# Kernel optimization log

Measured on AMD Instinct MI355X. Metric: run time of the kernel, lower is better.

The kernel has to match this reference:

```python
import jax, jax.numpy as jnp
import numpy as np
from jax import lax

B, C, H, W = 8, 128, 128, 128
K = 3
RED = 8

def setup_inputs() -> dict:
    key = jax.random.key(0)
    ks = jax.random.split(key, 8)
    s = 0.05
    return {
        "x": jax.random.normal(ks[0], (B, C, H, W), dtype=jnp.float32),
        "altitude": jax.random.normal(ks[1], (B, 128), dtype=jnp.float32),
        "W1": jax.random.normal(ks[2], (128, 128), dtype=jnp.float32) * s,          # Linear(128,128), no bias
        "W2": jax.random.normal(ks[3], (128 * K * K, 128), dtype=jnp.float32) * s,  # Linear(128,128*k*k)
        "conv_w": jax.random.normal(ks[4], (C, C), dtype=jnp.float32) * s,          # 1x1 conv weight [out,in]
        "conv_b": jax.random.normal(ks[5], (C,), dtype=jnp.float32) * s,
        "ca_w1": jax.random.normal(ks[6], (C // RED, C), dtype=jnp.float32) * s,    # CA squeeze 1x1 conv
        "ca_w2": jax.random.normal(ks[7], (C, C // RED), dtype=jnp.float32) * s,    # CA excite 1x1 conv
    }

def reference(x, altitude, W1, W2, conv_w, conv_b, ca_w1, ca_w2):
    b, c, h, w = x.shape
    # kernel generator MLP: [b,128] -> [b, 128*K*K] -> (b*c, 1, K, K)
    feat = jax.nn.leaky_relu(altitude @ W1.T, negative_slope=0.1)
    kern = (feat @ W2.T).reshape(b * c, 1, K, K)
    # per-sample, per-channel conv: groups = b*c (pure generated depthwise)
    pad = (K - 1) // 2
    xr = x.reshape(1, b * c, h, w)
    out = lax.conv_general_dilated(
        xr, kern, window_strides=(1, 1), padding=[(pad, pad), (pad, pad)],
        dimension_numbers=("NCHW", "OIHW", "NCHW"), feature_group_count=b * c)
    out = jax.nn.relu(out).reshape(b, c, h, w)
    # 1x1 pointwise conv
    out = jnp.einsum("bchw,oc->bohw", out, conv_w) + conv_b[None, :, None, None]
    # channel attention from altitude
    a1 = jax.nn.leaky_relu(altitude @ ca_w1.T, negative_slope=0.1)
    att = jax.nn.sigmoid(a1 @ ca_w2.T)  # [b, c]
    return out + x * att[:, :, None, None]
```

## Files before the change

kernel.cpp:

```cpp
#include <hip/hip_runtime.h>
#include <math.h>

typedef __attribute__((ext_vector_type(8))) __bf16 bf16x8;
typedef __attribute__((ext_vector_type(4))) __bf16 bf16x4;
typedef __attribute__((ext_vector_type(4))) float f32x4;

#define PLANE 16384
#define ROWW 128


__global__ __launch_bounds__(256) void precompute_kernel(
    const float* __restrict__ altitude,
    const float* __restrict__ W1,
    const float* __restrict__ W2,
    const float* __restrict__ ca_w1,
    const float* __restrict__ ca_w2,
    const float* __restrict__ conv_w,
    float* __restrict__ ws)
{
    int bid = blockIdx.x;
    int b = bid >> 2;
    int q = bid & 3;
    int t = threadIdx.x;
    __shared__ float alt_s[128];
    __shared__ float feat_s[128];
    __shared__ float a1_s[16];

    if (t < 128) alt_s[t] = altitude[b * 128 + t];
    __syncthreads();

    if (t < 128) {
        float s = 0.f;
        const float* wrow = W1 + t * 128;
        for (int j = 0; j < 128; ++j) s += alt_s[j] * wrow[j];
        feat_s[t] = (s >= 0.f) ? s : 0.1f * s;
    } else if (t < 144 && q == 1) {
        int r = t - 128;
        float s = 0.f;
        const float* wrow = ca_w1 + r * 128;
        for (int j = 0; j < 128; ++j) s += alt_s[j] * wrow[j];
        a1_s[r] = (s >= 0.f) ? s : 0.1f * s;
    }
    __syncthreads();

    for (int i = t; i < 288; i += 256) {
        int m = q * 288 + i;
        float s = 0.f;
        const float* wrow = W2 + m * 128;
        for (int j = 0; j < 128; ++j) s += feat_s[j] * wrow[j];
        int c = m / 9, k = m % 9;
        ws[b * 1536 + c * 12 + k] = s;
    }
    if (q == 1 && t < 128) {
        float s = 0.f;
        const float* wrow = ca_w2 + t * 16;
        for (int r = 0; r < 16; ++r) s += a1_s[r] * wrow[r];
        ws[12288 + b * 128 + t] = 1.f / (1.f + expf(-s));
    }
    if (q == 2 && t < 256) {
        int kc   = t >> 6;
        int lane = t & 63;
        int o  = b * 16 + (lane & 15);
        int cb = kc * 32 + 8 * (lane >> 4);
        bf16x8 v;
        #pragma unroll
        for (int j = 0; j < 8; ++j)
            v[j] = (__bf16)conv_w[o * 128 + cb + j];
        ushort* wf = (ushort*)(ws + 13312);
        *reinterpret_cast<bf16x8*>(wf + ((size_t)(b * 4 + kc) * 64 + lane) * 8) = v;
    }
}

__global__ __launch_bounds__(512, 4) void fused_kernel(
    const float* __restrict__ x,
    const float* __restrict__ conv_b,
    const float* __restrict__ ws,
    float* __restrict__ out)
{
    const float* __restrict__ kern_w = ws;
    const float* __restrict__ att_w  = ws + 12288;
    const ushort* __restrict__ wfrag = (const ushort*)(ws + 13312);

    int bid = blockIdx.x;
    int b  = bid & 7;
    int rb = bid >> 3;
    int h0 = rb * 2;

    __shared__ __align__(16) ushort dwT[2][128 * 136];
    __shared__ __align__(16) float ktaps[128 * 12];

    int t = threadIdx.x;
    const float* __restrict__ xb = x + (size_t)b * 128 * PLANE;

    for (int i = t; i < 384; i += 512) {
        float4 v = *(const float4*)(kern_w + b * 1536 + i * 4);
        *(float4*)(&ktaps[i * 4]) = v;
    }
    __syncthreads();

    {
        int pg = t & 15;
        int cg = t >> 4;
        int gp0 = pg * 8;
        int c0 = cg * 4;

        float mL = (pg > 0)  ? 1.f : 0.f;
        float mR = (pg < 15) ? 1.f : 0.f;
        float mTop = (rb > 0)  ? 1.f : 0.f;
        float mBot = (rb < 63) ? 1.f : 0.f;
        int r0 = (rb > 0)  ? h0 - 1 : h0;
        int r3 = (rb < 63) ? h0 + 2 : h0;

        bf16x4 bv[2][8];

#define NEIGH(A, B, LV, RV) \
        float LV = __shfl_up((B).w, 1) * mL; \
        float RV = __shfl_down((A).x, 1) * mR;

#define ROWACC(A, B, LV, RV, KL, KC, KR) {                                \
        o0 = fmaf((KL), LV,    fmaf((KC), (A).x, fmaf((KR), (A).y, o0))); \
        o1 = fmaf((KL), (A).x, fmaf((KC), (A).y, fmaf((KR), (A).z, o1))); \
        o2 = fmaf((KL), (A).y, fmaf((KC), (A).z, fmaf((KR), (A).w, o2))); \
        o3 = fmaf((KL), (A).z, fmaf((KC), (A).w, fmaf((KR), (B).x, o3))); \
        o4 = fmaf((KL), (A).w, fmaf((KC), (B).x, fmaf((KR), (B).y, o4))); \
        o5 = fmaf((KL), (B).x, fmaf((KC), (B).y, fmaf((KR), (B).z, o5))); \
        o6 = fmaf((KL), (B).y, fmaf((KC), (B).z, fmaf((KR), (B).w, o6))); \
        o7 = fmaf((KL), (B).z, fmaf((KC), (B).w, fmaf((KR), RV,    o7))); }

#define DW_CH(CI) {                                                    \
        const float* q_ = xb + (size_t)(c0 + (CI)) * PLANE;            \
        const float* p0_ = q_ + r0 * ROWW + gp0;                       \
        const float* p1_ = q_ + h0 * ROWW + gp0;                       \
        const float* p2_ = q_ + (h0 + 1) * ROWW + gp0;                 \
        const float* p3_ = q_ + r3 * ROWW + gp0;                       \
        float4 a0 = *(const float4*)p0_, b0 = *(const float4*)(p0_ + 4); \
        float4 a1 = *(const float4*)p1_, b1 = *(const float4*)(p1_ + 4); \
        float4 a2 = *(const float4*)p2_, b2 = *(const float4*)(p2_ + 4); \
        float4 a3 = *(const float4*)p3_, b3 = *(const float4*)(p3_ + 4); \
        NEIGH(a0, b0, l0, rr0) NEIGH(a1, b1, l1, rr1)                  \
        NEIGH(a2, b2, l2, rr2) NEIGH(a3, b3, l3, rr3)                  \
        const float* tp = ktaps + (c0 + (CI)) * 12;                    \
        float4 kA = *(const float4*)tp;                                \
        float4 kB = *(const float4*)(tp + 4);                          \
        float  k8v = tp[8];                                            \
        {            \
            float o0 = 0.f, o1 = 0.f, o2 = 0.f, o3 = 0.f;              \
            float o4 = 0.f, o5 = 0.f, o6 = 0.f, o7 = 0.f;              \
            ROWACC(a0, b0, l0, rr0, kA.x * mTop, kA.y * mTop, kA.z * mTop) \
            ROWACC(a1, b1, l1, rr1, kA.w, kB.x, kB.y)                  \
            ROWACC(a2, b2, l2, rr2, kB.z, kB.w, k8v)                   \
            bv[0][0][(CI)] = (__bf16)fmaxf(o0, 0.f);                   \
            bv[0][1][(CI)] = (__bf16)fmaxf(o1, 0.f);                   \
            bv[0][2][(CI)] = (__bf16)fmaxf(o2, 0.f);                   \
            bv[0][3][(CI)] = (__bf16)fmaxf(o3, 0.f);                   \
            bv[0][4][(CI)] = (__bf16)fmaxf(o4, 0.f);                   \
            bv[0][5][(CI)] = (__bf16)fmaxf(o5, 0.f);                   \
            bv[0][6][(CI)] = (__bf16)fmaxf(o6, 0.f);                   \
            bv[0][7][(CI)] = (__bf16)fmaxf(o7, 0.f);                   \
        }                                                              \
        {         \
            float o0 = 0.f, o1 = 0.f, o2 = 0.f, o3 = 0.f;              \
            float o4 = 0.f, o5 = 0.f, o6 = 0.f, o7 = 0.f;              \
            ROWACC(a1, b1, l1, rr1, kA.x, kA.y, kA.z)                  \
            ROWACC(a2, b2, l2, rr2, kA.w, kB.x, kB.y)                  \
            ROWACC(a3, b3, l3, rr3, kB.z * mBot, kB.w * mBot, k8v * mBot) \
            bv[1][0][(CI)] = (__bf16)fmaxf(o0, 0.f);                   \
            bv[1][1][(CI)] = (__bf16)fmaxf(o1, 0.f);                   \
            bv[1][2][(CI)] = (__bf16)fmaxf(o2, 0.f);                   \
            bv[1][3][(CI)] = (__bf16)fmaxf(o3, 0.f);                   \
            bv[1][4][(CI)] = (__bf16)fmaxf(o4, 0.f);                   \
            bv[1][5][(CI)] = (__bf16)fmaxf(o5, 0.f);                   \
            bv[1][6][(CI)] = (__bf16)fmaxf(o6, 0.f);                   \
            bv[1][7][(CI)] = (__bf16)fmaxf(o7, 0.f);                   \
        } }

        DW_CH(0) DW_CH(1) DW_CH(2) DW_CH(3)
#undef DW_CH
#undef ROWACC
#undef NEIGH

        int slotoff = (((cg >> 1) ^ pg) * 8) + ((cg & 1) * 4);
#define ST(RW, J) *reinterpret_cast<bf16x4*>(&dwT[RW][(pg * 8 + (J)) * 136 + slotoff]) = bv[RW][J];
        ST(0,0) ST(0,1) ST(0,2) ST(0,3) ST(0,4) ST(0,5) ST(0,6) ST(0,7)
        ST(1,0) ST(1,1) ST(1,2) ST(1,3) ST(1,4) ST(1,5) ST(1,6) ST(1,7)
#undef ST
    }
    __syncthreads();
    __builtin_amdgcn_sched_barrier(0);

    {
        int w    = t >> 6;
        int lane = t & 63;
        int r = lane & 15;
        int g = lane >> 4;

        bf16x8 bfr[4];
        #pragma unroll
        for (int kc = 0; kc < 4; ++kc)
            bfr[kc] = *reinterpret_cast<const bf16x8*>(
                wfrag + ((size_t)(w * 4 + kc) * 64 + lane) * 8);

        int o = w * 16 + r;
        float bi = conv_b[o];
        float at = att_w[b * 128 + o];

        #pragma unroll 1
        for (int r2 = 0; r2 < 2; ++r2) {
            const ushort* plane = dwT[r2];
            size_t rowoff = (size_t)(b * 128 + o) * PLANE + (size_t)(h0 + r2) * ROWW;
            const float* xrow = x + rowoff;
            float* orow = out + rowoff;

            float4 xv[8];
            #pragma unroll
            for (int pt = 0; pt < 8; ++pt)
                xv[pt] = *(const float4*)(xrow + pt * 16 + g * 4);

            f32x4 acc[8];
            #pragma unroll
            for (int pt = 0; pt < 8; ++pt) acc[pt] = (f32x4){0.f, 0.f, 0.f, 0.f};

            #pragma unroll
            for (int pt = 0; pt < 8; ++pt) {
                int px = pt * 16 + r;
                int srow = px * 136;
                int s2 = px >> 3;
                #pragma unroll
                for (int kc = 0; kc < 4; ++kc) {
                    bf16x8 a = *reinterpret_cast<const bf16x8*>(
                        &plane[srow + (((kc * 4 + g) ^ s2) * 8)]);
                    acc[pt] = __builtin_amdgcn_mfma_f32_16x16x32_bf16(a, bfr[kc], acc[pt], 0, 0, 0);
                }
            }

            #pragma unroll
            for (int pt = 0; pt < 8; ++pt) {
                int px = pt * 16 + g * 4;
                float4 ov;
                ov.x = acc[pt][0] + bi + xv[pt].x * at;
                ov.y = acc[pt][1] + bi + xv[pt].y * at;
                ov.z = acc[pt][2] + bi + xv[pt].z * at;
                ov.w = acc[pt][3] + bi + xv[pt].w * at;
                *(float4*)(orow + px) = ov;
            }
        }
    }
}

extern "C" void kernel_launch(void* const* d_in, const int* in_sizes, int n_in,
                              void* d_out, int out_size, void* d_ws, size_t ws_size,
                              hipStream_t stream) {
    (void)in_sizes; (void)n_in; (void)out_size; (void)ws_size;
    const float* x        = (const float*)d_in[0];
    const float* altitude = (const float*)d_in[1];
    const float* W1       = (const float*)d_in[2];
    const float* W2       = (const float*)d_in[3];
    const float* conv_w   = (const float*)d_in[4];
    const float* conv_b   = (const float*)d_in[5];
    const float* ca_w1    = (const float*)d_in[6];
    const float* ca_w2    = (const float*)d_in[7];
    float* out = (float*)d_out;
    float* ws  = (float*)d_ws;

    hipLaunchKernelGGL(precompute_kernel, dim3(32), dim3(256), 0, stream,
                       altitude, W1, W2, ca_w1, ca_w2, conv_w, ws);
    hipLaunchKernelGGL(fused_kernel, dim3(512), dim3(512), 0, stream,
                       x, conv_b, ws, out);
}
```

Measured before the change: 44.78 us.

## Restructure depthwise stage so each lane loads two rows and shares middle rows via shuffles

Changes the depthwise conv thread mapping: each wave handles 16 channels, with half-waves owning the two output rows and each lane covering 4 pixels. Every lane loads only two input rows per channel, and the middle row comes from a cross-half xor shuffle, replacing the four-row loads per thread. This is meant to cut redundant global loads and register pressure. It adds more shuffles, and the launch bound's minimum-blocks hint drops from 4 to 2, which loosens the register cap.

Measured after the change: 46.28 us. 3.4% more time.

```diff
diff --git a/kernel.cpp b/kernel.cpp
--- a/kernel.cpp
+++ b/kernel.cpp
@@ -71,7 +71,7 @@
     }
 }
 
-__global__ __launch_bounds__(512, 4) void fused_kernel(
+__global__ __launch_bounds__(512, 2) void fused_kernel(
     const float* __restrict__ x,
     const float* __restrict__ conv_b,
     const float* __restrict__ ws,
@@ -99,91 +99,82 @@
     __syncthreads();
 
     {
-        int pg = t & 15;
-        int cg = t >> 4;
-        int gp0 = pg * 8;
-        int c0 = cg * 4;
-
-        float mL = (pg > 0)  ? 1.f : 0.f;
-        float mR = (pg < 15) ? 1.f : 0.f;
-        float mTop = (rb > 0)  ? 1.f : 0.f;
-        float mBot = (rb < 63) ? 1.f : 0.f;
-        int r0 = (rb > 0)  ? h0 - 1 : h0;
-        int r3 = (rb < 63) ? h0 + 2 : h0;
-
-        bf16x4 bv[2][8];
-
-#define NEIGH(A, B, LV, RV) \
-        float LV = __shfl_up((B).w, 1) * mL; \
-        float RV = __shfl_down((A).x, 1) * mR;
-
-#define ROWACC(A, B, LV, RV, KL, KC, KR) {                                \
-        o0 = fmaf((KL), LV,    fmaf((KC), (A).x, fmaf((KR), (A).y, o0))); \
-        o1 = fmaf((KL), (A).x, fmaf((KC), (A).y, fmaf((KR), (A).z, o1))); \
-        o2 = fmaf((KL), (A).y, fmaf((KC), (A).z, fmaf((KR), (A).w, o2))); \
-        o3 = fmaf((KL), (A).z, fmaf((KC), (A).w, fmaf((KR), (B).x, o3))); \
-        o4 = fmaf((KL), (A).w, fmaf((KC), (B).x, fmaf((KR), (B).y, o4))); \
-        o5 = fmaf((KL), (B).x, fmaf((KC), (B).y, fmaf((KR), (B).z, o5))); \
-        o6 = fmaf((KL), (B).y, fmaf((KC), (B).z, fmaf((KR), (B).w, o6))); \
-        o7 = fmaf((KL), (B).z, fmaf((KC), (B).w, fmaf((KR), RV,    o7))); }
-
-#define DW_CH(CI) {                                                    \
-        const float* q_ = xb + (size_t)(c0 + (CI)) * PLANE;            \
-        const float* p0_ = q_ + r0 * ROWW + gp0;                       \
-        const float* p1_ = q_ + h0 * ROWW + gp0;                       \
-        const float* p2_ = q_ + (h0 + 1) * ROWW + gp0;                 \
-        const float* p3_ = q_ + r3 * ROWW + gp0;                       \
-        float4 a0 = *(const float4*)p0_, b0 = *(const float4*)(p0_ + 4); \
-        float4 a1 = *(const float4*)p1_, b1 = *(const float4*)(p1_ + 4); \
-        float4 a2 = *(const float4*)p2_, b2 = *(const float4*)(p2_ + 4); \
-        float4 a3 = *(const float4*)p3_, b3 = *(const float4*)(p3_ + 4); \
-        NEIGH(a0, b0, l0, rr0) NEIGH(a1, b1, l1, rr1)                  \
-        NEIGH(a2, b2, l2, rr2) NEIGH(a3, b3, l3, rr3)                  \
-        const float* tp = ktaps + (c0 + (CI)) * 12;                    \
+        int lane = t & 63;
+        int wv   = t >> 6;
+        int half = lane >> 5;
+        int m32  = lane & 31;
+        int p0   = m32 * 4;
+
+        int rA  = half ? h0 : ((rb > 0) ? h0 - 1 : 0);
+        int rBr = half ? ((rb < 63) ? h0 + 2 : 127) : (h0 + 1);
+        float mTopL = (rb == 0  && half == 0) ? 0.f : 1.f;
+        float mBotL = (rb == 63 && half == 1) ? 0.f : 1.f;
+        float mLl = (m32 == 0)  ? 0.f : 1.f;
+        float mRl = (m32 == 31) ? 0.f : 1.f;
+
+        const float* baseA = xb + rA  * ROWW + p0;
+        const float* baseB = xb + rBr * ROWW + p0;
+
+        int c0w = wv * 16;
+        int pxg = m32 >> 1;
+
+#define CH_COMP(CB, CI, S0, S1, S2, S3) {                              \
+        size_t coff = (size_t)(c0w + (CB) + (CI)) * PLANE;             \
+        float4 vA = *(const float4*)(baseA + coff);                    \
+        float4 vB = *(const float4*)(baseB + coff);                    \
+        float4 tmp;                                                    \
+        tmp.x = half ? vA.x : vB.x; tmp.y = half ? vA.y : vB.y;        \
+        tmp.z = half ? vA.z : vB.z; tmp.w = half ? vA.w : vB.w;        \
+        float4 rM;                                                     \
+        rM.x = __shfl_xor(tmp.x, 32); rM.y = __shfl_xor(tmp.y, 32);    \
+        rM.z = __shfl_xor(tmp.z, 32); rM.w = __shfl_xor(tmp.w, 32);    \
+        const float* tp = ktaps + (c0w + (CB) + (CI)) * 12;            \
         float4 kA = *(const float4*)tp;                                \
         float4 kB = *(const float4*)(tp + 4);                          \
         float  k8v = tp[8];                                            \
-        {            \
-            float o0 = 0.f, o1 = 0.f, o2 = 0.f, o3 = 0.f;              \
-            float o4 = 0.f, o5 = 0.f, o6 = 0.f, o7 = 0.f;              \
-            ROWACC(a0, b0, l0, rr0, kA.x * mTop, kA.y * mTop, kA.z * mTop) \
-            ROWACC(a1, b1, l1, rr1, kA.w, kB.x, kB.y)                  \
-            ROWACC(a2, b2, l2, rr2, kB.z, kB.w, k8v)                   \
-            bv[0][0][(CI)] = (__bf16)fmaxf(o0, 0.f);                   \
-            bv[0][1][(CI)] = (__bf16)fmaxf(o1, 0.f);                   \
-            bv[0][2][(CI)] = (__bf16)fmaxf(o2, 0.f);                   \
-            bv[0][3][(CI)] = (__bf16)fmaxf(o3, 0.f);                   \
-            bv[0][4][(CI)] = (__bf16)fmaxf(o4, 0.f);                   \
-            bv[0][5][(CI)] = (__bf16)fmaxf(o5, 0.f);                   \
-            bv[0][6][(CI)] = (__bf16)fmaxf(o6, 0.f);                   \
-            bv[0][7][(CI)] = (__bf16)fmaxf(o7, 0.f);                   \
-        }                                                              \
-        {         \
-            float o0 = 0.f, o1 = 0.f, o2 = 0.f, o3 = 0.f;              \
-            float o4 = 0.f, o5 = 0.f, o6 = 0.f, o7 = 0.f;              \
-            ROWACC(a1, b1, l1, rr1, kA.x, kA.y, kA.z)                  \
-            ROWACC(a2, b2, l2, rr2, kA.w, kB.x, kB.y)                  \
-            ROWACC(a3, b3, l3, rr3, kB.z * mBot, kB.w * mBot, k8v * mBot) \
-            bv[1][0][(CI)] = (__bf16)fmaxf(o0, 0.f);                   \
-            bv[1][1][(CI)] = (__bf16)fmaxf(o1, 0.f);                   \
-            bv[1][2][(CI)] = (__bf16)fmaxf(o2, 0.f);                   \
-            bv[1][3][(CI)] = (__bf16)fmaxf(o3, 0.f);                   \
-            bv[1][4][(CI)] = (__bf16)fmaxf(o4, 0.f);                   \
-            bv[1][5][(CI)] = (__bf16)fmaxf(o5, 0.f);                   \
-            bv[1][6][(CI)] = (__bf16)fmaxf(o6, 0.f);                   \
-            bv[1][7][(CI)] = (__bf16)fmaxf(o7, 0.f);                   \
-        } }
-
-        DW_CH(0) DW_CH(1) DW_CH(2) DW_CH(3)
-#undef DW_CH
-#undef ROWACC
-#undef NEIGH
-
-        int slotoff = (((cg >> 1) ^ pg) * 8) + ((cg & 1) * 4);
-#define ST(RW, J) *reinterpret_cast<bf16x4*>(&dwT[RW][(pg * 8 + (J)) * 136 + slotoff]) = bv[RW][J];
-        ST(0,0) ST(0,1) ST(0,2) ST(0,3) ST(0,4) ST(0,5) ST(0,6) ST(0,7)
-        ST(1,0) ST(1,1) ST(1,2) ST(1,3) ST(1,4) ST(1,5) ST(1,6) ST(1,7)
-#undef ST
+        float kU0 = kA.x * mTopL, kU1 = kA.y * mTopL, kU2 = kA.z * mTopL; \
+        float kM0 = kA.w,         kM1 = kB.x,         kM2 = kB.y;      \
+        float kD0 = kB.z * mBotL, kD1 = kB.w * mBotL, kD2 = k8v * mBotL; \
+        float lU = __shfl_up(vA.w, 1) * mLl;                           \
+        float rU = __shfl_down(vA.x, 1) * mRl;                         \
+        float lM = __shfl_up(rM.w, 1) * mLl;                           \
+        float rMv = __shfl_down(rM.x, 1) * mRl;                        \
+        float lD = __shfl_up(vB.w, 1) * mLl;                           \
+        float rD = __shfl_down(vB.x, 1) * mRl;                         \
+        float o0 = fmaf(kU0, lU,   fmaf(kU1, vA.x, fmaf(kU2, vA.y,    \
+                   fmaf(kM0, lM,   fmaf(kM1, rM.x, fmaf(kM2, rM.y,    \
+                   fmaf(kD0, lD,   fmaf(kD1, vB.x, kD2 * vB.y))))))));\
+        float o1 = fmaf(kU0, vA.x, fmaf(kU1, vA.y, fmaf(kU2, vA.z,    \
+                   fmaf(kM0, rM.x, fmaf(kM1, rM.y, fmaf(kM2, rM.z,    \
+                   fmaf(kD0, vB.x, fmaf(kD1, vB.y, kD2 * vB.z))))))));\
+        float o2 = fmaf(kU0, vA.y, fmaf(kU1, vA.z, fmaf(kU2, vA.w,    \
+                   fmaf(kM0, rM.y, fmaf(kM1, rM.z, fmaf(kM2, rM.w,    \
+                   fmaf(kD0, vB.y, fmaf(kD1, vB.z, kD2 * vB.w))))))));\
+        float o3 = fmaf(kU0, vA.z, fmaf(kU1, vA.w, fmaf(kU2, rU,      \
+                   fmaf(kM0, rM.z, fmaf(kM1, rM.w, fmaf(kM2, rMv,     \
+                   fmaf(kD0, vB.z, fmaf(kD1, vB.w, kD2 * rD))))))));  \
+        S0[(CI)] = (__bf16)fmaxf(o0, 0.f);                             \
+        S1[(CI)] = (__bf16)fmaxf(o1, 0.f);                             \
+        S2[(CI)] = (__bf16)fmaxf(o2, 0.f);                             \
+        S3[(CI)] = (__bf16)fmaxf(o3, 0.f); }
+
+#define CH_GROUP(CB) {                                                 \
+        bf16x4 s0, s1, s2, s3;                                         \
+        CH_COMP(CB, 0, s0, s1, s2, s3)                                 \
+        CH_COMP(CB, 1, s0, s1, s2, s3)                                 \
+        CH_COMP(CB, 2, s0, s1, s2, s3)                                 \
+        CH_COMP(CB, 3, s0, s1, s2, s3)                                 \
+        int v_ = (c0w + (CB)) >> 3;                                    \
+        int soff_ = ((v_ ^ pxg) * 8) + ((c0w + (CB)) & 4);             \
+        ushort* dp_ = dwT[half];                                       \
+        *reinterpret_cast<bf16x4*>(&dp_[(p0 + 0) * 136 + soff_]) = s0; \
+        *reinterpret_cast<bf16x4*>(&dp_[(p0 + 1) * 136 + soff_]) = s1; \
+        *reinterpret_cast<bf16x4*>(&dp_[(p0 + 2) * 136 + soff_]) = s2; \
+        *reinterpret_cast<bf16x4*>(&dp_[(p0 + 3) * 136 + soff_]) = s3; }
+
+        CH_GROUP(0) CH_GROUP(4) CH_GROUP(8) CH_GROUP(12)
+#undef CH_GROUP
+#undef CH_COMP
     }
     __syncthreads();
     __builtin_amdgcn_sched_barrier(0);
```

## Process four rows per block with double-buffered depthwise tiles

Applied to the files above, without the earlier changes.

Each block now handles two 2-row bands (4 rows) instead of one, halving the grid to 256 blocks. B-fragment and tap loads are hoisted and shared across both bands. The depthwise results go into separate LDS buffers so the second band's depthwise can overlap the first band's MFMA stage. LDS usage doubles to about 140KB and the occupancy hint is dropped, which cuts blocks per CU to one and leaves fewer blocks than CUs.

New measurement: 54.32 us. +21.3%, slower.

```diff
diff --git a/kernel.cpp b/kernel.cpp
--- a/kernel.cpp
+++ b/kernel.cpp
@@ -7,6 +7,7 @@
 
 #define PLANE 16384
 #define ROWW 128
+#define DWPLANE (128 * 136)
 
 
 __global__ __launch_bounds__(256) void precompute_kernel(
@@ -71,7 +72,7 @@
     }
 }
 
-__global__ __launch_bounds__(512, 4) void fused_kernel(
+__global__ __launch_bounds__(512) void fused_kernel(
     const float* __restrict__ x,
     const float* __restrict__ conv_b,
     const float* __restrict__ ws,
@@ -81,13 +82,13 @@
     const float* __restrict__ att_w  = ws + 12288;
     const ushort* __restrict__ wfrag = (const ushort*)(ws + 13312);
 
-    int bid = blockIdx.x;
-    int b  = bid & 7;
-    int rb = bid >> 3;
-    int h0 = rb * 2;
-
-    __shared__ __align__(16) ushort dwT[2][128 * 136];
-    __shared__ __align__(16) float ktaps[128 * 12];
+    int bid  = blockIdx.x;
+    int b    = bid & 7;
+    int band = bid >> 3;
+    int hbase = band * 4;
+
+    __shared__ __align__(16) ushort dwT[2][2][DWPLANE];
+    __shared__ __align__(16) float ktaps[1536];
 
     int t = threadIdx.x;
     const float* __restrict__ xb = x + (size_t)b * 128 * PLANE;
@@ -98,18 +99,32 @@
     }
     __syncthreads();
 
-    {
-        int pg = t & 15;
-        int cg = t >> 4;
-        int gp0 = pg * 8;
-        int c0 = cg * 4;
-
-        float mL = (pg > 0)  ? 1.f : 0.f;
-        float mR = (pg < 15) ? 1.f : 0.f;
-        float mTop = (rb > 0)  ? 1.f : 0.f;
-        float mBot = (rb < 63) ? 1.f : 0.f;
-        int r0 = (rb > 0)  ? h0 - 1 : h0;
-        int r3 = (rb < 63) ? h0 + 2 : h0;
+    int pg = t & 15;
+    int cg = t >> 4;
+    int gp0 = pg * 8;
+    int c0 = cg * 4;
+    float mL = (pg > 0)  ? 1.f : 0.f;
+    float mR = (pg < 15) ? 1.f : 0.f;
+    int slotoff = (((cg >> 1) ^ pg) * 8) + ((cg & 1) * 4);
+    int w2   = t >> 6;
+    int lane = t & 63;
+    int r = lane & 15;
+    int g = lane >> 4;
+
+    bf16x8 bfr[4];
+    #pragma unroll
+    for (int kc = 0; kc < 4; ++kc)
+        bfr[kc] = *reinterpret_cast<const bf16x8*>(
+            wfrag + ((size_t)(w2 * 4 + kc) * 64 + lane) * 8);
+    int oo = w2 * 16 + r;
+    float bi = conv_b[oo];
+    float at = att_w[b * 128 + oo];
+
+    auto phase1 = [&](int h0, ushort* dst) {
+        float mTop = (h0 > 0)   ? 1.f : 0.f;
+        float mBot = (h0 < 126) ? 1.f : 0.f;
+        int r0 = (h0 > 0)   ? h0 - 1 : h0;
+        int r3 = (h0 < 126) ? h0 + 2 : h0 + 1;
 
         bf16x4 bv[2][8];
 
@@ -179,35 +194,17 @@
 #undef ROWACC
 #undef NEIGH
 
-        int slotoff = (((cg >> 1) ^ pg) * 8) + ((cg & 1) * 4);
-#define ST(RW, J) *reinterpret_cast<bf16x4*>(&dwT[RW][(pg * 8 + (J)) * 136 + slotoff]) = bv[RW][J];
+#define ST(RW, J) *reinterpret_cast<bf16x4*>(&dst[(RW) * DWPLANE + (pg * 8 + (J)) * 136 + slotoff]) = bv[RW][J];
         ST(0,0) ST(0,1) ST(0,2) ST(0,3) ST(0,4) ST(0,5) ST(0,6) ST(0,7)
         ST(1,0) ST(1,1) ST(1,2) ST(1,3) ST(1,4) ST(1,5) ST(1,6) ST(1,7)
 #undef ST
-    }
-    __syncthreads();
-    __builtin_amdgcn_sched_barrier(0);
-
-    {
-        int w    = t >> 6;
-        int lane = t & 63;
-        int r = lane & 15;
-        int g = lane >> 4;
-
-        bf16x8 bfr[4];
-        #pragma unroll
-        for (int kc = 0; kc < 4; ++kc)
-            bfr[kc] = *reinterpret_cast<const bf16x8*>(
-                wfrag + ((size_t)(w * 4 + kc) * 64 + lane) * 8);
-
-        int o = w * 16 + r;
-        float bi = conv_b[o];
-        float at = att_w[b * 128 + o];
-
+    };
+
+    auto phase2 = [&](int h0, const ushort* src) {
         #pragma unroll 1
         for (int r2 = 0; r2 < 2; ++r2) {
-            const ushort* plane = dwT[r2];
-            size_t rowoff = (size_t)(b * 128 + o) * PLANE + (size_t)(h0 + r2) * ROWW;
+            const ushort* plane = src + r2 * DWPLANE;
+            size_t rowoff = (size_t)(b * 128 + oo) * PLANE + (size_t)(h0 + r2) * ROWW;
             const float* xrow = x + rowoff;
             float* orow = out + rowoff;
 
@@ -244,7 +241,14 @@
                 *(float4*)(orow + px) = ov;
             }
         }
-    }
+    };
+
+    phase1(hbase, &dwT[0][0][0]);
+    __syncthreads();
+    phase2(hbase, &dwT[0][0][0]);
+    phase1(hbase + 2, &dwT[1][0][0]);
+    __syncthreads();
+    phase2(hbase + 2, &dwT[1][0][0]);
 }
 
 extern "C" void kernel_launch(void* const* d_in, const int* in_sizes, int n_in,
@@ -264,6 +268,6 @@
 
     hipLaunchKernelGGL(precompute_kernel, dim3(32), dim3(256), 0, stream,
                        altitude, W1, W2, ca_w1, ca_w2, conv_w, ws);
-    hipLaunchKernelGGL(fused_kernel, dim3(512), dim3(512), 0, stream,
+    hipLaunchKernelGGL(fused_kernel, dim3(256), dim3(512), 0, stream,
                        x, conv_b, ws, out);
 }
```

## Process four-row bands per block with 1024 threads to cut halo reloads

Applied to the files above, without the earlier changes.

Each block now covers four output rows instead of two, using 1024 threads, with each thread handling two channels across four rows. The depthwise stage loads six input rows per channel for four outputs instead of four rows for two, which cuts halo re-reads from global memory. Grid size is halved and shared memory grows to four bf16 planes (about 139KB), so only one block fits per CU and latency hiding depends on the 16 waves per block. The pointwise stage splits waves into output-tile and row-pair groups.

Measured after the change: 47.51 us. 1.06x slower.

```diff
diff --git a/kernel.cpp b/kernel.cpp
--- a/kernel.cpp
+++ b/kernel.cpp
@@ -2,11 +2,12 @@
 #include <math.h>
 
 typedef __attribute__((ext_vector_type(8))) __bf16 bf16x8;
-typedef __attribute__((ext_vector_type(4))) __bf16 bf16x4;
+typedef __attribute__((ext_vector_type(2))) __bf16 bf16x2;
 typedef __attribute__((ext_vector_type(4))) float f32x4;
 
 #define PLANE 16384
 #define ROWW 128
+#define DWPL 17408
 
 
 __global__ __launch_bounds__(256) void precompute_kernel(
@@ -71,7 +72,7 @@
     }
 }
 
-__global__ __launch_bounds__(512, 4) void fused_kernel(
+__global__ __launch_bounds__(1024, 4) void fused_kernel(
     const float* __restrict__ x,
     const float* __restrict__ conv_b,
     const float* __restrict__ ws,
@@ -81,20 +82,20 @@
     const float* __restrict__ att_w  = ws + 12288;
     const ushort* __restrict__ wfrag = (const ushort*)(ws + 13312);
 
-    int bid = blockIdx.x;
-    int b  = bid & 7;
-    int rb = bid >> 3;
-    int h0 = rb * 2;
-
-    __shared__ __align__(16) ushort dwT[2][128 * 136];
-    __shared__ __align__(16) float ktaps[128 * 12];
+    int bid  = blockIdx.x;
+    int b    = bid & 7;
+    int band = bid >> 3;
+    int h0 = band * 4;
+
+    __shared__ __align__(16) ushort dwT[4 * DWPL];
+    __shared__ __align__(16) float ktaps[1536];
 
     int t = threadIdx.x;
     const float* __restrict__ xb = x + (size_t)b * 128 * PLANE;
 
-    for (int i = t; i < 384; i += 512) {
-        float4 v = *(const float4*)(kern_w + b * 1536 + i * 4);
-        *(float4*)(&ktaps[i * 4]) = v;
+    if (t < 384) {
+        float4 v = *(const float4*)(kern_w + b * 1536 + t * 4);
+        *(float4*)(&ktaps[t * 4]) = v;
     }
     __syncthreads();
 
@@ -102,16 +103,16 @@
         int pg = t & 15;
         int cg = t >> 4;
         int gp0 = pg * 8;
-        int c0 = cg * 4;
+        int c0 = cg * 2;
 
         float mL = (pg > 0)  ? 1.f : 0.f;
         float mR = (pg < 15) ? 1.f : 0.f;
-        float mTop = (rb > 0)  ? 1.f : 0.f;
-        float mBot = (rb < 63) ? 1.f : 0.f;
-        int r0 = (rb > 0)  ? h0 - 1 : h0;
-        int r3 = (rb < 63) ? h0 + 2 : h0;
-
-        bf16x4 bv[2][8];
+        float mTop = (band > 0)  ? 1.f : 0.f;
+        float mBot = (band < 31) ? 1.f : 0.f;
+        int R0 = (band > 0)  ? h0 - 1 : h0;
+        int R5 = (band < 31) ? h0 + 4 : h0 + 3;
+
+        bf16x2 bv[4][8];
 
 #define NEIGH(A, B, LV, RV) \
         float LV = __shfl_up((B).w, 1) * mL; \
@@ -127,69 +128,67 @@
         o6 = fmaf((KL), (B).y, fmaf((KC), (B).z, fmaf((KR), (B).w, o6))); \
         o7 = fmaf((KL), (B).z, fmaf((KC), (B).w, fmaf((KR), RV,    o7))); }
 
+#define OUTROW(RW, CI, A0, B0, L0, R0v, A1, B1, L1, R1v, A2, B2, L2, R2v, KTm, KBm) { \
+        float o0 = 0.f, o1 = 0.f, o2 = 0.f, o3 = 0.f;                  \
+        float o4 = 0.f, o5 = 0.f, o6 = 0.f, o7 = 0.f;                  \
+        ROWACC(A0, B0, L0, R0v, kA.x * (KTm), kA.y * (KTm), kA.z * (KTm)) \
+        ROWACC(A1, B1, L1, R1v, kA.w, kB.x, kB.y)                      \
+        ROWACC(A2, B2, L2, R2v, kB.z * (KBm), kB.w * (KBm), k8v * (KBm)) \
+        bv[RW][0][(CI)] = (__bf16)fmaxf(o0, 0.f);                      \
+        bv[RW][1][(CI)] = (__bf16)fmaxf(o1, 0.f);                      \
+        bv[RW][2][(CI)] = (__bf16)fmaxf(o2, 0.f);                      \
+        bv[RW][3][(CI)] = (__bf16)fmaxf(o3, 0.f);                      \
+        bv[RW][4][(CI)] = (__bf16)fmaxf(o4, 0.f);                      \
+        bv[RW][5][(CI)] = (__bf16)fmaxf(o5, 0.f);                      \
+        bv[RW][6][(CI)] = (__bf16)fmaxf(o6, 0.f);                      \
+        bv[RW][7][(CI)] = (__bf16)fmaxf(o7, 0.f); }
+
 #define DW_CH(CI) {                                                    \
         const float* q_ = xb + (size_t)(c0 + (CI)) * PLANE;            \
-        const float* p0_ = q_ + r0 * ROWW + gp0;                       \
+        const float* p0_ = q_ + R0 * ROWW + gp0;                       \
         const float* p1_ = q_ + h0 * ROWW + gp0;                       \
         const float* p2_ = q_ + (h0 + 1) * ROWW + gp0;                 \
-        const float* p3_ = q_ + r3 * ROWW + gp0;                       \
+        const float* p3_ = q_ + (h0 + 2) * ROWW + gp0;                 \
+        const float* p4_ = q_ + (h0 + 3) * ROWW + gp0;                 \
+        const float* p5_ = q_ + R5 * ROWW + gp0;                       \
         float4 a0 = *(const float4*)p0_, b0 = *(const float4*)(p0_ + 4); \
         float4 a1 = *(const float4*)p1_, b1 = *(const float4*)(p1_ + 4); \
         float4 a2 = *(const float4*)p2_, b2 = *(const float4*)(p2_ + 4); \
         float4 a3 = *(const float4*)p3_, b3 = *(const float4*)(p3_ + 4); \
+        float4 a4 = *(const float4*)p4_, b4 = *(const float4*)(p4_ + 4); \
+        float4 a5 = *(const float4*)p5_, b5 = *(const float4*)(p5_ + 4); \
         NEIGH(a0, b0, l0, rr0) NEIGH(a1, b1, l1, rr1)                  \
         NEIGH(a2, b2, l2, rr2) NEIGH(a3, b3, l3, rr3)                  \
+        NEIGH(a4, b4, l4, rr4) NEIGH(a5, b5, l5, rr5)                  \
         const float* tp = ktaps + (c0 + (CI)) * 12;                    \
         float4 kA = *(const float4*)tp;                                \
         float4 kB = *(const float4*)(tp + 4);                          \
         float  k8v = tp[8];                                            \
-        {            \
-            float o0 = 0.f, o1 = 0.f, o2 = 0.f, o3 = 0.f;              \
-            float o4 = 0.f, o5 = 0.f, o6 = 0.f, o7 = 0.f;              \
-            ROWACC(a0, b0, l0, rr0, kA.x * mTop, kA.y * mTop, kA.z * mTop) \
-            ROWACC(a1, b1, l1, rr1, kA.w, kB.x, kB.y)                  \
-            ROWACC(a2, b2, l2, rr2, kB.z, kB.w, k8v)                   \
-            bv[0][0][(CI)] = (__bf16)fmaxf(o0, 0.f);                   \
-            bv[0][1][(CI)] = (__bf16)fmaxf(o1, 0.f);                   \
-            bv[0][2][(CI)] = (__bf16)fmaxf(o2, 0.f);                   \
-            bv[0][3][(CI)] = (__bf16)fmaxf(o3, 0.f);                   \
-            bv[0][4][(CI)] = (__bf16)fmaxf(o4, 0.f);                   \
-            bv[0][5][(CI)] = (__bf16)fmaxf(o5, 0.f);                   \
-            bv[0][6][(CI)] = (__bf16)fmaxf(o6, 0.f);                   \
-            bv[0][7][(CI)] = (__bf16)fmaxf(o7, 0.f);                   \
-        }                                                              \
-        {         \
-            float o0 = 0.f, o1 = 0.f, o2 = 0.f, o3 = 0.f;              \
-            float o4 = 0.f, o5 = 0.f, o6 = 0.f, o7 = 0.f;              \
-            ROWACC(a1, b1, l1, rr1, kA.x, kA.y, kA.z)                  \
-            ROWACC(a2, b2, l2, rr2, kA.w, kB.x, kB.y)                  \
-            ROWACC(a3, b3, l3, rr3, kB.z * mBot, kB.w * mBot, k8v * mBot) \
-            bv[1][0][(CI)] = (__bf16)fmaxf(o0, 0.f);                   \
-            bv[1][1][(CI)] = (__bf16)fmaxf(o1, 0.f);                   \
-            bv[1][2][(CI)] = (__bf16)fmaxf(o2, 0.f);                   \
-            bv[1][3][(CI)] = (__bf16)fmaxf(o3, 0.f);                   \
-            bv[1][4][(CI)] = (__bf16)fmaxf(o4, 0.f);                   \
-            bv[1][5][(CI)] = (__bf16)fmaxf(o5, 0.f);                   \
-            bv[1][6][(CI)] = (__bf16)fmaxf(o6, 0.f);                   \
-            bv[1][7][(CI)] = (__bf16)fmaxf(o7, 0.f);                   \
-        } }
-
-        DW_CH(0) DW_CH(1) DW_CH(2) DW_CH(3)
+        OUTROW(0, CI, a0, b0, l0, rr0, a1, b1, l1, rr1, a2, b2, l2, rr2, mTop, 1.f) \
+        OUTROW(1, CI, a1, b1, l1, rr1, a2, b2, l2, rr2, a3, b3, l3, rr3, 1.f, 1.f)  \
+        OUTROW(2, CI, a2, b2, l2, rr2, a3, b3, l3, rr3, a4, b4, l4, rr4, 1.f, 1.f)  \
+        OUTROW(3, CI, a3, b3, l3, rr3, a4, b4, l4, rr4, a5, b5, l5, rr5, 1.f, mBot) }
+
+        DW_CH(0) DW_CH(1)
 #undef DW_CH
+#undef OUTROW
 #undef ROWACC
 #undef NEIGH
 
-        int slotoff = (((cg >> 1) ^ pg) * 8) + ((cg & 1) * 4);
-#define ST(RW, J) *reinterpret_cast<bf16x4*>(&dwT[RW][(pg * 8 + (J)) * 136 + slotoff]) = bv[RW][J];
+        int slotoff = (((cg >> 2) ^ pg) * 8) + ((cg & 3) * 2);
+#define ST(RW, J) *reinterpret_cast<bf16x2*>(&dwT[(RW) * DWPL + (pg * 8 + (J)) * 136 + slotoff]) = bv[RW][J];
         ST(0,0) ST(0,1) ST(0,2) ST(0,3) ST(0,4) ST(0,5) ST(0,6) ST(0,7)
         ST(1,0) ST(1,1) ST(1,2) ST(1,3) ST(1,4) ST(1,5) ST(1,6) ST(1,7)
+        ST(2,0) ST(2,1) ST(2,2) ST(2,3) ST(2,4) ST(2,5) ST(2,6) ST(2,7)
+        ST(3,0) ST(3,1) ST(3,2) ST(3,3) ST(3,4) ST(3,5) ST(3,6) ST(3,7)
 #undef ST
     }
     __syncthreads();
-    __builtin_amdgcn_sched_barrier(0);
 
     {
         int w    = t >> 6;
+        int ot   = w >> 1;
+        int rp   = w & 1;
         int lane = t & 63;
         int r = lane & 15;
         int g = lane >> 4;
@@ -198,16 +197,17 @@
         #pragma unroll
         for (int kc = 0; kc < 4; ++kc)
             bfr[kc] = *reinterpret_cast<const bf16x8*>(
-                wfrag + ((size_t)(w * 4 + kc) * 64 + lane) * 8);
-
-        int o = w * 16 + r;
+                wfrag + ((size_t)(ot * 4 + kc) * 64 + lane) * 8);
+
+        int o = ot * 16 + r;
         float bi = conv_b[o];
         float at = att_w[b * 128 + o];
 
         #pragma unroll 1
         for (int r2 = 0; r2 < 2; ++r2) {
-            const ushort* plane = dwT[r2];
-            size_t rowoff = (size_t)(b * 128 + o) * PLANE + (size_t)(h0 + r2) * ROWW;
+            int row = rp * 2 + r2;
+            const ushort* plane = dwT + row * DWPL;
+            size_t rowoff = (size_t)(b * 128 + o) * PLANE + (size_t)(h0 + row) * ROWW;
             const float* xrow = x + rowoff;
             float* orow = out + rowoff;
 
@@ -264,6 +264,6 @@
 
     hipLaunchKernelGGL(precompute_kernel, dim3(32), dim3(256), 0, stream,
                        altitude, W1, W2, ca_w1, ca_w2, conv_w, ws);
-    hipLaunchKernelGGL(fused_kernel, dim3(512), dim3(512), 0, stream,
+    hipLaunchKernelGGL(fused_kernel, dim3(256), dim3(1024), 0, stream,
                        x, conv_b, ws, out);
 }
```
